# Kernel optimization log

Hardware: AMD Instinct MI355X
Metric: run time of the kernel (lower is better)

Reference implementation:

```python
import jax, jax.numpy as jnp
import numpy as np

HID = 256
SLOTS = 64
K = 2
TAU = 8.0
EPS = 1e-5


def setup_inputs() -> dict:
    key = jax.random.key(0)
    ks = jax.random.split(key, 8)
    B, T = 512, 256
    s = lambda fan_in: 1.0 / np.sqrt(fan_in)
    return {
        "x": jax.random.uniform(ks[0], (B, T, 1), jnp.float32, 0.0, 10.0),
        "W_embed": jax.random.uniform(ks[1], (HID, 1), jnp.float32, -1.0, 1.0),
        "b_embed": jax.random.uniform(ks[2], (HID,), jnp.float32, -1.0, 1.0),
        "W_update": jax.random.uniform(ks[3], (HID, HID), jnp.float32, -s(HID), s(HID)),
        "b_update": jax.random.uniform(ks[4], (HID,), jnp.float32, -s(HID), s(HID)),
        "gamma": jnp.ones((HID,), jnp.float32),
        "beta": jnp.zeros((HID,), jnp.float32),
        "W_out": jax.random.uniform(ks[5], (10, HID), jnp.float32, -s(HID), s(HID)),
        "b_out": jax.random.uniform(ks[6], (10,), jnp.float32, -s(HID), s(HID)),
        "context_strength": jnp.float32(0.2),
    }


def _gaussian_attention(pointer, num_positions):
    # pointer: [B] float. Returns indices [B,5] int32, weights [B,5] float.
    offsets = jnp.arange(-K, K + 1)
    base = jnp.clip(jnp.floor(pointer).astype(jnp.int32), 0, num_positions - 1)
    indices = (base[:, None] + offsets[None, :]) % num_positions
    delta = indices.astype(pointer.dtype) - pointer[:, None]
    weights = jax.nn.softmax(-(delta ** 2) / TAU, axis=1)
    return indices, weights


def reference(x, W_embed, b_embed, W_update, b_update, gamma, beta, W_out, b_out, context_strength):
    B, T, _ = x.shape
    cs = jax.nn.sigmoid(context_strength)

    def step(carry, x_t):
        h, memory, pointer = carry  # [B,H], [B,SLOTS,H], [B]
        inp = jnp.tanh(x_t @ W_embed.T + b_embed)           # [B,H]
        indices, weights = _gaussian_attention(pointer, SLOTS)
        neighborhood = jnp.take_along_axis(memory, indices[:, :, None], axis=1)  # [B,5,H]
        context = jnp.einsum('bk,bkh->bh', weights, neighborhood)
        combined = inp + cs * context
        h = jnp.tanh((combined + h) @ W_update.T + b_update)
        mu = jnp.mean(h, axis=-1, keepdims=True)
        var = jnp.mean((h - mu) ** 2, axis=-1, keepdims=True)
        h = (h - mu) * jax.lax.rsqrt(var + EPS) * gamma + beta
        contribution = weights[:, :, None] * h[:, None, :]   # [B,5,H]
        memory = jax.vmap(lambda m, i, c: m.at[i].add(c))(memory, indices, contribution)
        pointer = (pointer + 1.0) % SLOTS
        return (h, memory, pointer), None

    h0 = jnp.zeros((B, HID), x.dtype)
    mem0 = jnp.zeros((B, SLOTS, HID), x.dtype)
    ptr0 = jnp.zeros((B,), x.dtype)
    (h, _, _), _ = jax.lax.scan(step, (h0, mem0, ptr0), jnp.swapaxes(x, 0, 1))
    return h @ W_out.T + b_out
```

## Files before the change

### kernel.cpp

```cpp
#include <hip/hip_runtime.h>


#define TT 256

typedef __bf16 bf16x8 __attribute__((ext_vector_type(8)));
typedef float  f32x4  __attribute__((ext_vector_type(4)));

__device__ __forceinline__ float fast_tanh(float x) {
    float e = __expf(2.f * x);
    return 1.f - __fdividef(2.f, e + 1.f);
}

template<int CTRL, int RM>
__device__ __forceinline__ float dpp_add(float v) {
    int t = __builtin_amdgcn_update_dpp(0, __float_as_int(v), CTRL, RM, 0xf, true);
    return v + __int_as_float(t);
}
__device__ __forceinline__ float wave_sum63(float v) {
    v = dpp_add<0xB1,  0xf>(v);
    v = dpp_add<0x4E,  0xf>(v);
    v = dpp_add<0x141, 0xf>(v);
    v = dpp_add<0x140, 0xf>(v);
    v = dpp_add<0x142, 0xa>(v);
    v = dpp_add<0x143, 0xc>(v);
    return v;
}

#define SMEM_BYTES 138512

__global__ __launch_bounds__(512, 2)
void postnorm_kernel(const float* __restrict__ x,
                     const float* __restrict__ W_embed,
                     const float* __restrict__ b_embed,
                     const float* __restrict__ W_update,
                     const float* __restrict__ b_update,
                     const float* __restrict__ gamma,
                     const float* __restrict__ beta,
                     const float* __restrict__ W_out,
                     const float* __restrict__ b_out,
                     const float* __restrict__ ctx_s,
                     float* __restrict__ out)
{
    extern __shared__ __align__(16) char smem[];
    float*  s_mem  = (float*)(smem);
    float*  s_x    = (float*)(smem + 131072);
    float*  s_y    = (float*)(smem + 133120);
    __bf16* s_v    = (__bf16*)(smem + 135168);
    float*  s_red1 = (float*)(smem + 136320);
    float*  s_red2 = (float*)(smem + 136352);
    float*  s_wt   = (float*)(smem + 136384);
    float*  s_oacc = (float*)(smem + 138432);

    const int tid  = threadIdx.x;
    const int n    = tid >> 8;
    const int i    = tid & 255;
    const int wave = tid >> 6;
    const int lane = tid & 63;
    const int bn   = lane & 15;
    const int quad = lane >> 4;
    const int r0   = blockIdx.x * 2;

    {   f32x4 z = {0.f, 0.f, 0.f, 0.f};
        f32x4* p = (f32x4*)s_mem;
        #pragma unroll
        for (int k = 0; k < 16; ++k) p[tid + k * 512] = z;
    }
    s_x[tid] = x[(r0 + n) * TT + i];
    if (tid < 20) s_oacc[tid] = 0.f;

    if (tid < 64) {
        float wv[5]; float ssum = 0.f;
        #pragma unroll
        for (int k = 0; k < 5; ++k) {
            int idx = (tid + k - 2) & 63;
            float d = (float)idx - (float)tid;
            wv[k] = expf(-(d * d) * 0.125f);
            ssum += wv[k];
        }
        #pragma unroll
        for (int k = 0; k < 5; ++k) s_wt[tid * 8 + k] = wv[k] / ssum;
    }

    const float we  = W_embed[i];
    const float be  = b_embed[i];
    const float bu  = b_update[i];
    const float gm  = gamma[i];
    const float btt = beta[i];
    const float csv = 1.f / (1.f + expf(-ctx_s[0]));

    bf16x8 wfa[2][8];
    #pragma unroll
    for (int mt = 0; mt < 2; ++mt) {
        #pragma unroll
        for (int kt = 0; kt < 8; ++kt) {
            const float* wp = W_update + (wave * 32 + mt * 16 + bn) * 256
                                       + kt * 32 + quad * 8;
            f32x4 a = *(const f32x4*)wp;
            f32x4 b = *(const f32x4*)(wp + 4);
            bf16x8 f;
            f[0] = (__bf16)a[0]; f[1] = (__bf16)a[1];
            f[2] = (__bf16)a[2]; f[3] = (__bf16)a[3];
            f[4] = (__bf16)b[0]; f[5] = (__bf16)b[1];
            f[6] = (__bf16)b[2]; f[7] = (__bf16)b[3];
            wfa[mt][kt] = f;
        }
    }

    __syncthreads();
    {
        float inp0 = fast_tanh(s_x[n * 256] * we + be);
        s_v[n * 288 + i] = (__bf16)inp0;
    }

    float wt0, wt1, wt2, wt3, wt4;
    {   f32x4 wv = *(const f32x4*)(s_wt);
        wt0 = wv[0]; wt1 = wv[1]; wt2 = wv[2]; wt3 = wv[3]; wt4 = s_wt[4];
    }
    f32x4 nw  = *(const f32x4*)(s_wt + 8);
    float nw4 = s_wt[8 + 4];
    float xn  = s_x[n * 256 + 1];
    float nf  = 0.f;
    __syncthreads();

    float hn = 0.f;
    float w0 = 0.f, w1 = 0.f, w2 = 0.f, w3 = 0.f, w4 = 0.f;
    float* mcol = s_mem + (n << 14) + i;
    const __bf16* vsrc = s_v + (bn & 1) * 288 + quad * 8;

    #pragma unroll 1
    for (int t = 0; t < TT; ++t) {
        float inp = fast_tanh(xn * we + be);

        f32x4 a0a = {0,0,0,0}, a0b = {0,0,0,0}, a1a = {0,0,0,0}, a1b = {0,0,0,0};
        #pragma unroll
        for (int kt = 0; kt < 4; ++kt) {
            bf16x8 bfr0 = *(const bf16x8*)(vsrc + kt * 32);
            bf16x8 bfr1 = *(const bf16x8*)(vsrc + (kt + 4) * 32);
            a0a = __builtin_amdgcn_mfma_f32_16x16x32_bf16(wfa[0][kt],     bfr0, a0a, 0, 0, 0);
            a1a = __builtin_amdgcn_mfma_f32_16x16x32_bf16(wfa[1][kt],     bfr0, a1a, 0, 0, 0);
            a0b = __builtin_amdgcn_mfma_f32_16x16x32_bf16(wfa[0][kt + 4], bfr1, a0b, 0, 0, 0);
            a1b = __builtin_amdgcn_mfma_f32_16x16x32_bf16(wfa[1][kt + 4], bfr1, a1b, 0, 0, 0);
        }
        if (bn < 2) {
            f32x4 y0 = a0a + a0b, y1 = a1a + a1b;
            float* yb = s_y + bn * 256 + wave * 32 + quad * 4;
            *(f32x4*)yb        = y0;
            *(f32x4*)(yb + 16) = y1;
        }
        __syncthreads();

        float yt = fast_tanh(s_y[tid] + bu);
        float s1 = wave_sum63(yt);
        float s2 = wave_sum63(yt * yt);
        if (lane == 63) { s_red1[wave] = s1; s_red2[wave] = s2; }
        __syncthreads();

        f32x4 r1 = *(const f32x4*)(s_red1 + n * 4);
        f32x4 r2 = *(const f32x4*)(s_red2 + n * 4);
        float S1 = (r1[0] + r1[1]) + (r1[2] + r1[3]);
        float S2 = (r2[0] + r2[1]) + (r2[2] + r2[3]);
        float mu   = S1 * (1.f / 256.f);
        float var  = S2 * (1.f / 256.f) - mu * mu;
        float rstd = rsqrtf(var + 1e-5f);
        hn = (yt - mu) * rstd * gm + btt;

        w0 += wt0 * hn; w1 += wt1 * hn; w2 += wt2 * hn;
        w3 += wt3 * hn; w4 += wt4 * hn;

        mcol[((t - 2) & 63) << 8] = w0;
        w0 = w1; w1 = w2; w2 = w3; w3 = w4; w4 = nf;
        float ctx = ((nw[0] * w0 + nw[1] * w1) + (nw[2] * w2 + nw[3] * w3))
                  + nw4 * w4;
        float v = inp + csv * ctx + hn;
        s_v[n * 288 + i] = (__bf16)v;
        wt0 = nw[0]; wt1 = nw[1]; wt2 = nw[2]; wt3 = nw[3]; wt4 = nw4;

        nf  = mcol[((t + 4) & 63) << 8];
        {   const float* wp = s_wt + ((t + 2) & 63) * 8;
            nw  = *(const f32x4*)wp;
            nw4 = wp[4];
        }
        xn  = s_x[n * 256 + ((t + 2) & 255)];
        __syncthreads();
    }

    #pragma unroll
    for (int o = 0; o < 10; ++o) {
        float p = hn * W_out[o * 256 + i];
        #pragma unroll
        for (int m = 32; m >= 1; m >>= 1) p += __shfl_xor(p, m, 64);
        if (lane == 0) atomicAdd(&s_oacc[n * 10 + o], p);
    }
    __syncthreads();
    if (tid < 20) {
        int nn = tid / 10, o = tid % 10;
        out[(r0 + nn) * 10 + o] = s_oacc[tid] + b_out[o];
    }
}

extern "C" void kernel_launch(void* const* d_in, const int* in_sizes, int n_in,
                              void* d_out, int out_size, void* d_ws, size_t ws_size,
                              hipStream_t stream) {
    const float* x    = (const float*)d_in[0];
    const float* W_e  = (const float*)d_in[1];
    const float* b_e  = (const float*)d_in[2];
    const float* W_u  = (const float*)d_in[3];
    const float* b_u  = (const float*)d_in[4];
    const float* gmm  = (const float*)d_in[5];
    const float* bta  = (const float*)d_in[6];
    const float* W_o  = (const float*)d_in[7];
    const float* b_o  = (const float*)d_in[8];
    const float* cst  = (const float*)d_in[9];
    float* out = (float*)d_out;

    (void)hipFuncSetAttribute(reinterpret_cast<const void*>(postnorm_kernel),
                              hipFuncAttributeMaxDynamicSharedMemorySize,
                              SMEM_BYTES);

    postnorm_kernel<<<dim3(256), dim3(512), SMEM_BYTES, stream>>>(
        x, W_e, b_e, W_u, b_u, gmm, bta, W_o, b_o, cst, out);
}
```

Measured before the change: 327.3 us.

## Move per-step elementwise/LayerNorm work to two waves with 4 features per lane

```diff
diff --git a/kernel.cpp b/kernel.cpp
--- a/kernel.cpp
+++ b/kernel.cpp
@@ -4,6 +4,7 @@
 #define TT 256
 
 typedef __bf16 bf16x8 __attribute__((ext_vector_type(8)));
+typedef __bf16 bf16x4 __attribute__((ext_vector_type(4)));
 typedef float  f32x4  __attribute__((ext_vector_type(4)));
 
 __device__ __forceinline__ float fast_tanh(float x) {
@@ -16,17 +17,18 @@
     int t = __builtin_amdgcn_update_dpp(0, __float_as_int(v), CTRL, RM, 0xf, true);
     return v + __int_as_float(t);
 }
-__device__ __forceinline__ float wave_sum63(float v) {
+__device__ __forceinline__ float wave_sum_all(float v) {
     v = dpp_add<0xB1,  0xf>(v);
     v = dpp_add<0x4E,  0xf>(v);
     v = dpp_add<0x141, 0xf>(v);
     v = dpp_add<0x140, 0xf>(v);
-    v = dpp_add<0x142, 0xa>(v);
-    v = dpp_add<0x143, 0xc>(v);
+    {   int t = __builtin_amdgcn_ds_swizzle(__float_as_int(v), 0x401F);
+        v += __int_as_float(t); }
+    v += __shfl_xor(v, 32, 64);
     return v;
 }
 
-#define SMEM_BYTES 138512
+#define SMEM_BYTES 138368
 
 __global__ __launch_bounds__(512, 2)
 void postnorm_kernel(const float* __restrict__ x,
@@ -42,31 +44,27 @@
                      float* __restrict__ out)
 {
     extern __shared__ __align__(16) char smem[];
-    float*  s_mem  = (float*)(smem);
-    float*  s_x    = (float*)(smem + 131072);
-    float*  s_y    = (float*)(smem + 133120);
-    __bf16* s_v    = (__bf16*)(smem + 135168);
-    float*  s_red1 = (float*)(smem + 136320);
-    float*  s_red2 = (float*)(smem + 136352);
-    float*  s_wt   = (float*)(smem + 136384);
-    float*  s_oacc = (float*)(smem + 138432);
+    float*  s_mem = (float*)(smem);
+    float*  s_x   = (float*)(smem + 131072);
+    float*  s_y   = (float*)(smem + 133120);
+    __bf16* s_v   = (__bf16*)(smem + 135168);
+    float*  s_wt  = (float*)(smem + 136320);
 
     const int tid  = threadIdx.x;
-    const int n    = tid >> 8;
-    const int i    = tid & 255;
     const int wave = tid >> 6;
     const int lane = tid & 63;
     const int bn   = lane & 15;
     const int quad = lane >> 4;
     const int r0   = blockIdx.x * 2;
+    const int n    = wave;
+    const int h0   = lane << 2;
 
     {   f32x4 z = {0.f, 0.f, 0.f, 0.f};
         f32x4* p = (f32x4*)s_mem;
         #pragma unroll
         for (int k = 0; k < 16; ++k) p[tid + k * 512] = z;
     }
-    s_x[tid] = x[(r0 + n) * TT + i];
-    if (tid < 20) s_oacc[tid] = 0.f;
+    s_x[tid] = x[(r0 + (tid >> 8)) * TT + (tid & 255)];
 
     if (tid < 64) {
         float wv[5]; float ssum = 0.f;
@@ -81,11 +79,6 @@
         for (int k = 0; k < 5; ++k) s_wt[tid * 8 + k] = wv[k] / ssum;
     }
 
-    const float we  = W_embed[i];
-    const float be  = b_embed[i];
-    const float bu  = b_update[i];
-    const float gm  = gamma[i];
-    const float btt = beta[i];
     const float csv = 1.f / (1.f + expf(-ctx_s[0]));
 
     bf16x8 wfa[2][8];
@@ -107,31 +100,54 @@
     }
 
     __syncthreads();
-    {
-        float inp0 = fast_tanh(s_x[n * 256] * we + be);
-        s_v[n * 288 + i] = (__bf16)inp0;
-    }
-
-    float wt0, wt1, wt2, wt3, wt4;
-    {   f32x4 wv = *(const f32x4*)(s_wt);
-        wt0 = wv[0]; wt1 = wv[1]; wt2 = wv[2]; wt3 = wv[3]; wt4 = s_wt[4];
-    }
-    f32x4 nw  = *(const f32x4*)(s_wt + 8);
-    float nw4 = s_wt[8 + 4];
-    float xn  = s_x[n * 256 + 1];
-    float nf  = 0.f;
+
+    f32x4 z4 = {0.f, 0.f, 0.f, 0.f};
+    f32x4 we = z4, be = z4, bu = z4, gm = z4, bt = z4;
+    f32x4 nw = z4, nf = z4, hn = z4;
+    f32x4 wr0 = z4, wr1 = z4, wr2 = z4, wr3 = z4, wr4 = z4;
+    float wt0 = 0.f, wt1 = 0.f, wt2 = 0.f, wt3 = 0.f, wt4 = 0.f;
+    float nw4 = 0.f, xn = 0.f;
+    float* mcol = s_mem;
+
+    if (wave < 2) {
+        we = *(const f32x4*)(W_embed  + h0);
+        be = *(const f32x4*)(b_embed  + h0);
+        bu = *(const f32x4*)(b_update + h0);
+        gm = *(const f32x4*)(gamma    + h0);
+        bt = *(const f32x4*)(beta     + h0);
+        mcol = s_mem + (n << 14) + h0;
+        float x0 = s_x[n * 256];
+        bf16x4 vv;
+        #pragma unroll
+        for (int j = 0; j < 4; ++j)
+            vv[j] = (__bf16)fast_tanh(x0 * we[j] + be[j]);
+        *(bf16x4*)(s_v + n * 288 + h0) = vv;
+        wt0 = s_wt[0]; wt1 = s_wt[1]; wt2 = s_wt[2]; wt3 = s_wt[3]; wt4 = s_wt[4];
+        nw  = *(const f32x4*)(s_wt + 8);
+        nw4 = s_wt[12];
+        xn  = s_x[n * 256 + 1];
+    }
     __syncthreads();
 
-    float hn = 0.f;
-    float w0 = 0.f, w1 = 0.f, w2 = 0.f, w3 = 0.f, w4 = 0.f;
-    float* mcol = s_mem + (n << 14) + i;
     const __bf16* vsrc = s_v + (bn & 1) * 288 + quad * 8;
 
     #pragma unroll 1
     for (int t = 0; t < TT; ++t) {
-        float inp = fast_tanh(xn * we + be);
-
-        f32x4 a0a = {0,0,0,0}, a0b = {0,0,0,0}, a1a = {0,0,0,0}, a1b = {0,0,0,0};
+        f32x4 base = z4;
+        float coef = 1.f;
+        if (wave < 2) {
+            float wdot = (nw[0] * wt1 + nw[1] * wt2)
+                       + (nw[2] * wt3 + nw[3] * wt4);
+            coef = 1.f + csv * wdot;
+            #pragma unroll
+            for (int j = 0; j < 4; ++j) {
+                float ctxA = ((nw[0] * wr1[j] + nw[1] * wr2[j])
+                            + (nw[2] * wr3[j] + nw[3] * wr4[j])) + nw4 * nf[j];
+                base[j] = fast_tanh(xn * we[j] + be[j]) + csv * ctxA;
+            }
+        }
+
+        f32x4 a0a = z4, a0b = z4, a1a = z4, a1b = z4;
         #pragma unroll
         for (int kt = 0; kt < 4; ++kt) {
             bf16x8 bfr0 = *(const bf16x8*)(vsrc + kt * 32);
@@ -149,52 +165,58 @@
         }
         __syncthreads();
 
-        float yt = fast_tanh(s_y[tid] + bu);
-        float s1 = wave_sum63(yt);
-        float s2 = wave_sum63(yt * yt);
-        if (lane == 63) { s_red1[wave] = s1; s_red2[wave] = s2; }
+        if (wave < 2) {
+            f32x4 yv = *(const f32x4*)(s_y + n * 256 + h0);
+            f32x4 yt;
+            #pragma unroll
+            for (int j = 0; j < 4; ++j) yt[j] = fast_tanh(yv[j] + bu[j]);
+            float ps1 = (yt[0] + yt[1]) + (yt[2] + yt[3]);
+            float ps2 = (yt[0]*yt[0] + yt[1]*yt[1]) + (yt[2]*yt[2] + yt[3]*yt[3]);
+            float S1 = wave_sum_all(ps1);
+            float S2 = wave_sum_all(ps2);
+            float mu   = S1 * (1.f / 256.f);
+            float var  = S2 * (1.f / 256.f) - mu * mu;
+            float rstd = rsqrtf(var + 1e-5f);
+            bf16x4 vv;
+            #pragma unroll
+            for (int j = 0; j < 4; ++j) {
+                hn[j] = (yt[j] - mu) * rstd * gm[j] + bt[j];
+                vv[j] = (__bf16)(base[j] + coef * hn[j]);
+            }
+            *(bf16x4*)(s_v + n * 288 + h0) = vv;
+
+            f32x4 ret;
+            #pragma unroll
+            for (int j = 0; j < 4; ++j) {
+                ret[j] = wr0[j] + wt0 * hn[j];
+                wr0[j] = wr1[j] + wt1 * hn[j];
+                wr1[j] = wr2[j] + wt2 * hn[j];
+                wr2[j] = wr3[j] + wt3 * hn[j];
+                wr3[j] = wr4[j] + wt4 * hn[j];
+                wr4[j] = nf[j];
+            }
+            *(f32x4*)(mcol + ((t - 2) & 63) * 256) = ret;
+            wt0 = nw[0]; wt1 = nw[1]; wt2 = nw[2]; wt3 = nw[3]; wt4 = nw4;
+            nf = *(const f32x4*)(mcol + ((t + 4) & 63) * 256);
+            {   const float* wp = s_wt + ((t + 2) & 63) * 8;
+                nw  = *(const f32x4*)wp;
+                nw4 = wp[4];
+            }
+            xn = s_x[n * 256 + ((t + 2) & 255)];
+        }
         __syncthreads();
-
-        f32x4 r1 = *(const f32x4*)(s_red1 + n * 4);
-        f32x4 r2 = *(const f32x4*)(s_red2 + n * 4);
-        float S1 = (r1[0] + r1[1]) + (r1[2] + r1[3]);
-        float S2 = (r2[0] + r2[1]) + (r2[2] + r2[3]);
-        float mu   = S1 * (1.f / 256.f);
-        float var  = S2 * (1.f / 256.f) - mu * mu;
-        float rstd = rsqrtf(var + 1e-5f);
-        hn = (yt - mu) * rstd * gm + btt;
-
-        w0 += wt0 * hn; w1 += wt1 * hn; w2 += wt2 * hn;
-        w3 += wt3 * hn; w4 += wt4 * hn;
-
-        mcol[((t - 2) & 63) << 8] = w0;
-        w0 = w1; w1 = w2; w2 = w3; w3 = w4; w4 = nf;
-        float ctx = ((nw[0] * w0 + nw[1] * w1) + (nw[2] * w2 + nw[3] * w3))
-                  + nw4 * w4;
-        float v = inp + csv * ctx + hn;
-        s_v[n * 288 + i] = (__bf16)v;
-        wt0 = nw[0]; wt1 = nw[1]; wt2 = nw[2]; wt3 = nw[3]; wt4 = nw4;
-
-        nf  = mcol[((t + 4) & 63) << 8];
-        {   const float* wp = s_wt + ((t + 2) & 63) * 8;
-            nw  = *(const f32x4*)wp;
-            nw4 = wp[4];
-        }
-        xn  = s_x[n * 256 + ((t + 2) & 255)];
-        __syncthreads();
-    }
-
-    #pragma unroll
-    for (int o = 0; o < 10; ++o) {
-        float p = hn * W_out[o * 256 + i];
-        #pragma unroll
-        for (int m = 32; m >= 1; m >>= 1) p += __shfl_xor(p, m, 64);
-        if (lane == 0) atomicAdd(&s_oacc[n * 10 + o], p);
-    }
-    __syncthreads();
-    if (tid < 20) {
-        int nn = tid / 10, o = tid % 10;
-        out[(r0 + nn) * 10 + o] = s_oacc[tid] + b_out[o];
+    }
+
+    if (wave < 2) {
+        #pragma unroll
+        for (int o = 0; o < 10; ++o) {
+            f32x4 wo = *(const f32x4*)(W_out + o * 256 + h0);
+            float p = (hn[0] * wo[0] + hn[1] * wo[1])
+                    + (hn[2] * wo[2] + hn[3] * wo[3]);
+            #pragma unroll
+            for (int m = 32; m >= 1; m >>= 1) p += __shfl_xor(p, m, 64);
+            if (lane == 0) out[(r0 + n) * 10 + o] = p + b_out[o];
+        }
     }
 }
 
```

After: 363.6 us. 11.1% more time.

## Remap thread ownership to MFMA output lanes, removing s_y staging and a barrier

Applied to the files above, without the earlier changes.

```diff
diff --git a/kernel.cpp b/kernel.cpp
--- a/kernel.cpp
+++ b/kernel.cpp
@@ -16,17 +16,13 @@
     int t = __builtin_amdgcn_update_dpp(0, __float_as_int(v), CTRL, RM, 0xf, true);
     return v + __int_as_float(t);
 }
-__device__ __forceinline__ float wave_sum63(float v) {
-    v = dpp_add<0xB1,  0xf>(v);
-    v = dpp_add<0x4E,  0xf>(v);
-    v = dpp_add<0x141, 0xf>(v);
-    v = dpp_add<0x140, 0xf>(v);
-    v = dpp_add<0x142, 0xa>(v);
-    v = dpp_add<0x143, 0xc>(v);
-    return v;
-}
-
-#define SMEM_BYTES 138512
+template<int IMM>
+__device__ __forceinline__ float swz_add(float v) {
+    int t = __builtin_amdgcn_ds_swizzle(__float_as_int(v), IMM);
+    return v + __int_as_float(t);
+}
+
+#define SMEM_BYTES 136528
 
 __global__ __launch_bounds__(512, 2)
 void postnorm_kernel(const float* __restrict__ x,
@@ -44,28 +40,29 @@
     extern __shared__ __align__(16) char smem[];
     float*  s_mem  = (float*)(smem);
     float*  s_x    = (float*)(smem + 131072);
-    float*  s_y    = (float*)(smem + 133120);
-    __bf16* s_v    = (__bf16*)(smem + 135168);
-    float*  s_red1 = (float*)(smem + 136320);
-    float*  s_red2 = (float*)(smem + 136352);
-    float*  s_wt   = (float*)(smem + 136384);
-    float*  s_oacc = (float*)(smem + 138432);
+    __bf16* s_v    = (__bf16*)(smem + 133120);
+    float*  s_red1 = (float*)(smem + 134272);
+    float*  s_red2 = (float*)(smem + 134336);
+    float*  s_wt   = (float*)(smem + 134400);
+    float*  s_oacc = (float*)(smem + 136448);
 
     const int tid  = threadIdx.x;
-    const int n    = tid >> 8;
-    const int i    = tid & 255;
     const int wave = tid >> 6;
     const int lane = tid & 63;
     const int bn   = lane & 15;
     const int quad = lane >> 4;
     const int r0   = blockIdx.x * 2;
 
+    const int b     = bn >> 1;
+    const int row   = bn & 1;
+    const int i_own = wave * 32 + (b >> 2) * 16 + quad * 4 + (b & 3);
+
     {   f32x4 z = {0.f, 0.f, 0.f, 0.f};
         f32x4* p = (f32x4*)s_mem;
         #pragma unroll
         for (int k = 0; k < 16; ++k) p[tid + k * 512] = z;
     }
-    s_x[tid] = x[(r0 + n) * TT + i];
+    s_x[tid] = x[(r0 + (tid >> 8)) * TT + (tid & 255)];
     if (tid < 20) s_oacc[tid] = 0.f;
 
     if (tid < 64) {
@@ -81,11 +78,11 @@
         for (int k = 0; k < 5; ++k) s_wt[tid * 8 + k] = wv[k] / ssum;
     }
 
-    const float we  = W_embed[i];
-    const float be  = b_embed[i];
-    const float bu  = b_update[i];
-    const float gm  = gamma[i];
-    const float btt = beta[i];
+    const float we  = W_embed[i_own];
+    const float be  = b_embed[i_own];
+    const float bu  = b_update[i_own];
+    const float gm  = gamma[i_own];
+    const float btt = beta[i_own];
     const float csv = 1.f / (1.f + expf(-ctx_s[0]));
 
     bf16x8 wfa[2][8];
@@ -96,20 +93,20 @@
             const float* wp = W_update + (wave * 32 + mt * 16 + bn) * 256
                                        + kt * 32 + quad * 8;
             f32x4 a = *(const f32x4*)wp;
-            f32x4 b = *(const f32x4*)(wp + 4);
+            f32x4 bb = *(const f32x4*)(wp + 4);
             bf16x8 f;
-            f[0] = (__bf16)a[0]; f[1] = (__bf16)a[1];
-            f[2] = (__bf16)a[2]; f[3] = (__bf16)a[3];
-            f[4] = (__bf16)b[0]; f[5] = (__bf16)b[1];
-            f[6] = (__bf16)b[2]; f[7] = (__bf16)b[3];
+            f[0] = (__bf16)a[0];  f[1] = (__bf16)a[1];
+            f[2] = (__bf16)a[2];  f[3] = (__bf16)a[3];
+            f[4] = (__bf16)bb[0]; f[5] = (__bf16)bb[1];
+            f[6] = (__bf16)bb[2]; f[7] = (__bf16)bb[3];
             wfa[mt][kt] = f;
         }
     }
 
     __syncthreads();
     {
-        float inp0 = fast_tanh(s_x[n * 256] * we + be);
-        s_v[n * 288 + i] = (__bf16)inp0;
+        float inp0 = fast_tanh(s_x[row * 256] * we + be);
+        s_v[row * 288 + i_own] = (__bf16)inp0;
     }
 
     float wt0, wt1, wt2, wt3, wt4;
@@ -118,14 +115,14 @@
     }
     f32x4 nw  = *(const f32x4*)(s_wt + 8);
     float nw4 = s_wt[8 + 4];
-    float xn  = s_x[n * 256 + 1];
+    float xn  = s_x[row * 256 + 1];
     float nf  = 0.f;
     __syncthreads();
 
     float hn = 0.f;
     float w0 = 0.f, w1 = 0.f, w2 = 0.f, w3 = 0.f, w4 = 0.f;
-    float* mcol = s_mem + (n << 14) + i;
-    const __bf16* vsrc = s_v + (bn & 1) * 288 + quad * 8;
+    float* mcol = s_mem + (row << 14) + i_own;
+    const __bf16* vsrc = s_v + row * 288 + quad * 8;
 
     #pragma unroll 1
     for (int t = 0; t < TT; ++t) {
@@ -141,24 +138,34 @@
             a0b = __builtin_amdgcn_mfma_f32_16x16x32_bf16(wfa[0][kt + 4], bfr1, a0b, 0, 0, 0);
             a1b = __builtin_amdgcn_mfma_f32_16x16x32_bf16(wfa[1][kt + 4], bfr1, a1b, 0, 0, 0);
         }
-        if (bn < 2) {
-            f32x4 y0 = a0a + a0b, y1 = a1a + a1b;
-            float* yb = s_y + bn * 256 + wave * 32 + quad * 4;
-            *(f32x4*)yb        = y0;
-            *(f32x4*)(yb + 16) = y1;
+
+        f32x4 y0 = a0a + a0b, y1 = a1a + a1b;
+        f32x4 ym = (b & 4) ? y1 : y0;
+        float yA = (b & 2) ? ym[2] : ym[0];
+        float yB = (b & 2) ? ym[3] : ym[1];
+        float ysel = (b & 1) ? yB : yA;
+
+        float yt = fast_tanh(ysel + bu);
+        float s1 = yt, s2 = yt * yt;
+        s1 = dpp_add<0x4E, 0xf>(s1);  s2 = dpp_add<0x4E, 0xf>(s2);
+        s1 = swz_add<0x101F>(s1);     s2 = swz_add<0x101F>(s2);
+        s1 = swz_add<0x201F>(s1);     s2 = swz_add<0x201F>(s2);
+        s1 = swz_add<0x401F>(s1);     s2 = swz_add<0x401F>(s2);
+        s1 += __shfl_xor(s1, 32, 64); s2 += __shfl_xor(s2, 32, 64);
+        if (lane < 2) {
+            s_red1[lane * 8 + wave] = s1;
+            s_red2[lane * 8 + wave] = s2;
         }
         __syncthreads();
 
-        float yt = fast_tanh(s_y[tid] + bu);
-        float s1 = wave_sum63(yt);
-        float s2 = wave_sum63(yt * yt);
-        if (lane == 63) { s_red1[wave] = s1; s_red2[wave] = s2; }
-        __syncthreads();
-
-        f32x4 r1 = *(const f32x4*)(s_red1 + n * 4);
-        f32x4 r2 = *(const f32x4*)(s_red2 + n * 4);
-        float S1 = (r1[0] + r1[1]) + (r1[2] + r1[3]);
-        float S2 = (r2[0] + r2[1]) + (r2[2] + r2[3]);
+        f32x4 r1a = *(const f32x4*)(s_red1 + row * 8);
+        f32x4 r1b = *(const f32x4*)(s_red1 + row * 8 + 4);
+        f32x4 r2a = *(const f32x4*)(s_red2 + row * 8);
+        f32x4 r2b = *(const f32x4*)(s_red2 + row * 8 + 4);
+        float S1 = ((r1a[0] + r1a[1]) + (r1a[2] + r1a[3]))
+                 + ((r1b[0] + r1b[1]) + (r1b[2] + r1b[3]));
+        float S2 = ((r2a[0] + r2a[1]) + (r2a[2] + r2a[3]))
+                 + ((r2b[0] + r2b[1]) + (r2b[2] + r2b[3]));
         float mu   = S1 * (1.f / 256.f);
         float var  = S2 * (1.f / 256.f) - mu * mu;
         float rstd = rsqrtf(var + 1e-5f);
@@ -172,7 +179,7 @@
         float ctx = ((nw[0] * w0 + nw[1] * w1) + (nw[2] * w2 + nw[3] * w3))
                   + nw4 * w4;
         float v = inp + csv * ctx + hn;
-        s_v[n * 288 + i] = (__bf16)v;
+        s_v[row * 288 + i_own] = (__bf16)v;
         wt0 = nw[0]; wt1 = nw[1]; wt2 = nw[2]; wt3 = nw[3]; wt4 = nw4;
 
         nf  = mcol[((t + 4) & 63) << 8];
@@ -180,16 +187,22 @@
             nw  = *(const f32x4*)wp;
             nw4 = wp[4];
         }
-        xn  = s_x[n * 256 + ((t + 2) & 255)];
+        xn  = s_x[row * 256 + ((t + 2) & 255)];
         __syncthreads();
     }
 
-    #pragma unroll
-    for (int o = 0; o < 10; ++o) {
-        float p = hn * W_out[o * 256 + i];
-        #pragma unroll
-        for (int m = 32; m >= 1; m >>= 1) p += __shfl_xor(p, m, 64);
-        if (lane == 0) atomicAdd(&s_oacc[n * 10 + o], p);
+    s_x[row * 256 + i_own] = hn;
+    __syncthreads();
+    {
+        const int n = tid >> 8, i = tid & 255;
+        float h = s_x[tid];
+        #pragma unroll
+        for (int o = 0; o < 10; ++o) {
+            float p = h * W_out[o * 256 + i];
+            #pragma unroll
+            for (int m = 32; m >= 1; m >>= 1) p += __shfl_xor(p, m, 64);
+            if (lane == 0) atomicAdd(&s_oacc[n * 10 + o], p);
+        }
     }
     __syncthreads();
     if (tid < 20) {
```

Result: faster. 310.7 us (-5.0%).
